# Optimization experiments

Measured on AMD Instinct MI355X. Metric: run time of the kernel, lower is better.

## Reference

```python
import jax, jax.numpy as jnp
import numpy as np

B, N_IN, N_HID, N_OUT, N_CLUST = 4096, 32, 128, 30000, 10000
BN_EPS = 1e-3  # scvi FCLayers uses BatchNorm1d(eps=0.001)


def setup_inputs() -> dict:
    key = jax.random.key(0)
    ks = jax.random.split(key, 4)
    z = jax.random.normal(ks[0], (B, N_IN), dtype=jnp.float32)
    W1 = jax.random.normal(ks[1], (N_HID, N_IN), dtype=jnp.float32) * 0.1
    b1 = jnp.zeros((N_HID,), dtype=jnp.float32)
    gamma = jnp.ones((N_HID,), dtype=jnp.float32)
    beta = jnp.zeros((N_HID,), dtype=jnp.float32)
    W2 = jax.random.normal(ks[2], (N_OUT, N_HID), dtype=jnp.float32) * 0.05
    b2 = jnp.zeros((N_OUT,), dtype=jnp.float32)
    # 3 introns per cluster, sorted cluster ids; first intron of each cluster
    intron_clusters = (jnp.arange(N_OUT, dtype=jnp.int32) // 3).astype(jnp.int32)
    first_indices = (jnp.arange(N_CLUST, dtype=jnp.int32) * 3).astype(jnp.int32)
    return {"z": z, "W1": W1, "b1": b1, "gamma": gamma, "beta": beta,
            "W2": W2, "b2": b2, "intron_clusters": intron_clusters,
            "first_indices": first_indices}


def reference(z, W1, b1, gamma, beta, W2, b2, intron_clusters, first_indices):
    # FCLayers (1 layer, dropout=0): Linear -> BatchNorm1d (batch stats) -> ReLU
    h = z @ W1.T + b1                                   # [B, n_hidden]
    mu = jnp.mean(h, axis=0)
    var = jnp.var(h, axis=0)
    h = gamma * (h - mu) * jax.lax.rsqrt(var + BN_EPS) + beta
    h = jax.nn.relu(h)
    # second_part Linear
    potentials = h @ W2.T + b2                          # [B, n_output]
    # pin first intron of each cluster to 0 (scatter-zero mask)
    potentials = potentials.at[:, first_indices].set(0.0)
    p_u = jnp.exp(potentials)                           # [B, n_output]
    # sparse cluster_summation @ p_u.T  ==  segment sum over introns per cluster
    cluster_sums = jax.ops.segment_sum(p_u.T, intron_clusters,
                                       num_segments=N_CLUST).T  # [B, n_clusters]
    # gather each intron's cluster sum and normalize (segment softmax)
    norm_factor = cluster_sums[:, intron_clusters]      # [B, n_output]
    return p_u / norm_factor
```

## Files before the change

### kernel.cpp

```cpp
#include <hip/hip_runtime.h>
#include <hip/hip_bf16.h>


typedef float  floatx4 __attribute__((ext_vector_type(4)));
typedef __bf16 bf16x8  __attribute__((ext_vector_type(8)));
typedef __bf16 bf16x4  __attribute__((ext_vector_type(4)));

struct F3 { float x, y, z; };

#define GLOBAL_AS __attribute__((address_space(1)))
#define LDS_AS    __attribute__((address_space(3)))

__device__ __forceinline__ void async16(void* lds, const void* g) {
    __builtin_amdgcn_global_load_lds((const GLOBAL_AS void*)g, (LDS_AS void*)lds, 16, 0, 0);
}

__global__ __launch_bounds__(256) void k_hidden_cvt(const float* __restrict__ z,
                                                    const float* __restrict__ W1,
                                                    const float* __restrict__ b1,
                                                    float* __restrict__ h,
                                                    float* __restrict__ stats,
                                                    const float* __restrict__ w2,
                                                    __bf16* __restrict__ w2b) {
    const int bid = blockIdx.x;
    const int tid = threadIdx.x;
    if (bid >= 256) {
        const int i  = (bid - 256) * 256 + tid;
        const int rp = i >> 4;
        const int c  = i & 15;
        const int nb = rp >> 5, n = rp & 31;
        const int src = nb * 48 + 3 * (n & 15) + 1 + (n >> 4);
        const float* s = w2 + (size_t)src * 128 + c * 8;
        floatx4 v0 = *(const floatx4*)s;
        floatx4 v1 = *(const floatx4*)(s + 4);
        bf16x8 o;
        o[0] = (__bf16)v0[0]; o[1] = (__bf16)v0[1]; o[2] = (__bf16)v0[2]; o[3] = (__bf16)v0[3];
        o[4] = (__bf16)v1[0]; o[5] = (__bf16)v1[1]; o[6] = (__bf16)v1[2]; o[7] = (__bf16)v1[3];
        *(bf16x8*)(w2b + (size_t)rp * 128 + c * 8) = o;
        return;
    }
    __shared__ float sW1[128 * 33];
    __shared__ float sz[16 * 32];
    __shared__ float red[256];
    const int rb = bid * 16;
    for (int i = tid; i < 128 * 32; i += 256) sW1[(i >> 5) * 33 + (i & 31)] = W1[i];
    for (int i = tid; i < 16 * 32; i += 256) sz[i] = z[rb * 32 + i];
    __syncthreads();
    const int col = tid & 127, rh = tid >> 7;
    const float bias = b1[col];
    float lsum = 0.f, lsq = 0.f;
    for (int r = rh; r < 16; r += 2) {
        float acc = bias;
#pragma unroll
        for (int k = 0; k < 32; ++k) acc += sz[r * 32 + k] * sW1[col * 33 + k];
        h[(rb + r) * 128 + col] = acc;
        lsum += acc; lsq += acc * acc;
    }
    red[tid] = lsum; __syncthreads();
    if (rh == 0) atomicAdd(&stats[col], red[col] + red[col + 128]);
    __syncthreads();
    red[tid] = lsq; __syncthreads();
    if (rh == 0) atomicAdd(&stats[128 + col], red[col] + red[col + 128]);
}

__global__ __launch_bounds__(256) void k_norm(const float* __restrict__ h,
                                              const float* __restrict__ stats,
                                              const float* __restrict__ gamma,
                                              const float* __restrict__ beta,
                                              __bf16* __restrict__ hb) {
    const int idx = blockIdx.x * 256 + threadIdx.x;
    const int c0  = (idx * 4) & 127;
    floatx4 v = *(const floatx4*)(h + (size_t)idx * 4);
    bf16x4 o;
#pragma unroll
    for (int j = 0; j < 4; ++j) {
        const int col = c0 + j;
        const float mu  = stats[col] * (1.0f / 4096.0f);
        const float var = stats[128 + col] * (1.0f / 4096.0f) - mu * mu;
        const float sc  = gamma[col] * rsqrtf(var + 1e-3f);
        const float sh  = beta[col] - mu * sc;
        o[j] = (__bf16)fmaxf(v[j] * sc + sh, 0.0f);
    }
    *(bf16x4*)(hb + (size_t)idx * 4) = o;
}

__global__ __launch_bounds__(256, 3) void k_main(const __bf16* __restrict__ hb,
                                                 const __bf16* __restrict__ w2b,
                                                 const float* __restrict__ b2,
                                                 float* __restrict__ out) {
    __shared__ __align__(16) char smem[32768 + 2 * 8192];
    char* smemA = smem;
    const int tid    = threadIdx.x;
    const int rowblk = blockIdx.x & 31;
    const int slot   = blockIdx.x >> 5;
    const int row0   = rowblk * 128;

    {
        const char* g = (const char*)(hb + (size_t)row0 * 128);
#pragma unroll
        for (int it = 0; it < 8; ++it) {
            int L = it * 256 + tid;
            int row = L >> 4, c = L & 15;
            int gc = (c & 8) | ((c ^ row) & 7);
            async16(smemA + L * 16, g + (row * 16 + gc) * 16);
        }
    }
    auto stageB = [&](char* dst, int nb) {
        const char* g = (const char*)(w2b + (size_t)nb * 32 * 128);
#pragma unroll
        for (int it = 0; it < 2; ++it) {
            int L = it * 256 + tid;
            int n = L >> 4, c = L & 15;
            int gc = (c & 8) | ((c ^ n) & 7);
            async16(dst + L * 16, g + (n * 16 + gc) * 16);
        }
    };
    stageB(smem + 32768, slot);

    const int lane = tid & 63, w = tid >> 6;
    const int quad = lane >> 4, lr = lane & 15;
    const int cnt = (624 - slot) / 24 + 1;
    __syncthreads();

    for (int i = 0; i < cnt; ++i) {
        const int nblk = slot + 24 * i;
        char* bcur  = smem + 32768 + ((i & 1) << 13);
        char* bnext = smem + 32768 + ((~i & 1) << 13);
        if (i + 1 < cnt) stageB(bnext, nblk + 24);

        const int cb = nblk * 48 + 3 * lr;
        const float bb1 = b2[cb + 1];
        const float bb2 = b2[cb + 2];

        const floatx4 z4 = {0.f, 0.f, 0.f, 0.f};
        floatx4 acc[2][2] = {{z4, z4}, {z4, z4}};
#pragma unroll
        for (int ks = 0; ks < 4; ++ks) {
            const int cg = ks * 4 + quad;
            bf16x8 a[2], b[2];
#pragma unroll
            for (int s = 0; s < 2; ++s) {
                int r  = w * 32 + s * 16 + lr;
                int ch = (cg & 8) | ((cg ^ r) & 7);
                a[s] = *(const bf16x8*)(smemA + r * 256 + ch * 16);
            }
#pragma unroll
            for (int t = 0; t < 2; ++t) {
                int n  = t * 16 + lr;
                int ch = (cg & 8) | ((cg ^ n) & 7);
                b[t] = *(const bf16x8*)(bcur + n * 256 + ch * 16);
            }
#pragma unroll
            for (int s = 0; s < 2; ++s)
#pragma unroll
                for (int t = 0; t < 2; ++t)
                    acc[s][t] = __builtin_amdgcn_mfma_f32_16x16x32_bf16(a[s], b[t], acc[s][t], 0, 0, 0);
        }

#pragma unroll
        for (int s = 0; s < 2; ++s) {
#pragma unroll
            for (int r = 0; r < 4; ++r) {
                int m = row0 + w * 32 + s * 16 + quad * 4 + r;
                float v1  = __expf(acc[s][0][r] + bb1);
                float v2  = __expf(acc[s][1][r] + bb2);
                float inv = __builtin_amdgcn_rcpf(1.0f + v1 + v2);
                F3 o; o.x = inv; o.y = v1 * inv; o.z = v2 * inv;
                *(F3*)(out + (size_t)m * 30000 + cb) = o;
            }
        }
        __syncthreads();
    }
}

extern "C" void kernel_launch(void* const* d_in, const int* in_sizes, int n_in,
                              void* d_out, int out_size, void* d_ws, size_t ws_size,
                              hipStream_t stream) {
    const float* z     = (const float*)d_in[0];
    const float* W1    = (const float*)d_in[1];
    const float* b1    = (const float*)d_in[2];
    const float* gamma = (const float*)d_in[3];
    const float* beta  = (const float*)d_in[4];
    const float* W2    = (const float*)d_in[5];
    const float* b2    = (const float*)d_in[6];
    float* out = (float*)d_out;

    char* ws = (char*)d_ws;
    float*  h     = (float*)ws;
    __bf16* hb    = (__bf16*)(ws + (2u << 20));
    __bf16* w2b   = (__bf16*)(ws + (3u << 20));
    float*  stats = (float*)(ws + (11u << 20));

    hipMemsetAsync(stats, 0, 256 * sizeof(float), stream);
    k_hidden_cvt<<<1506, 256, 0, stream>>>(z, W1, b1, h, stats, W2, w2b);
    k_norm<<<512, 256, 0, stream>>>(h, stats, gamma, beta, hb);
    k_main<<<768, 256, 0, stream>>>(hb, w2b, b2, out);
}
```

Baseline: 564.6 us.

## Replace persistent double-buffered B loop with one-shot 2D grid tiles

The main GEMM+softmax kernel drops its persistent loop over 24 slots with double-buffered W2 tiles. It now launches a 32x313 grid where each block loads its A tile and a 64-row W2 tile once, computes two cluster groups, and writes the output. This removes the per-iteration barrier and lets many more blocks hide store latency, but each block has to reload the 32KB A tile, which adds L2 traffic and launch overhead. The last column handles only one group.

```diff
diff --git a/kernel.cpp b/kernel.cpp
--- a/kernel.cpp
+++ b/kernel.cpp
@@ -88,12 +88,14 @@
                                                  const __bf16* __restrict__ w2b,
                                                  const float* __restrict__ b2,
                                                  float* __restrict__ out) {
-    __shared__ __align__(16) char smem[32768 + 2 * 8192];
+    __shared__ __align__(16) char smem[49152];
     char* smemA = smem;
+    char* smemB = smem + 32768;
     const int tid    = threadIdx.x;
-    const int rowblk = blockIdx.x & 31;
-    const int slot   = blockIdx.x >> 5;
+    const int rowblk = blockIdx.x;
+    const int y      = blockIdx.y;
     const int row0   = rowblk * 128;
+    const int ulim   = (y == 312) ? 1 : 2;
 
     {
         const char* g = (const char*)(hb + (size_t)row0 * 128);
@@ -105,71 +107,79 @@
             async16(smemA + L * 16, g + (row * 16 + gc) * 16);
         }
     }
-    auto stageB = [&](char* dst, int nb) {
-        const char* g = (const char*)(w2b + (size_t)nb * 32 * 128);
-#pragma unroll
-        for (int it = 0; it < 2; ++it) {
+    {
+        const char* g = (const char*)(w2b + (size_t)y * 64 * 128);
+#pragma unroll
+        for (int it = 0; it < 4; ++it) {
             int L = it * 256 + tid;
             int n = L >> 4, c = L & 15;
             int gc = (c & 8) | ((c ^ n) & 7);
-            async16(dst + L * 16, g + (n * 16 + gc) * 16);
-        }
-    };
-    stageB(smem + 32768, slot);
+            int nn = (n < 32 * ulim) ? n : (n - 32);
+            async16(smemB + L * 16, g + (nn * 16 + gc) * 16);
+        }
+    }
 
     const int lane = tid & 63, w = tid >> 6;
     const int quad = lane >> 4, lr = lane & 15;
-    const int cnt = (624 - slot) / 24 + 1;
+    const int cb0 = y * 96 + 3 * lr;
+    float bb1[2], bb2[2];
+    bb1[0] = b2[cb0 + 1]; bb2[0] = b2[cb0 + 2];
+    if (ulim > 1) { bb1[1] = b2[cb0 + 49]; bb2[1] = b2[cb0 + 50]; }
+    else          { bb1[1] = 0.f;          bb2[1] = 0.f; }
     __syncthreads();
 
-    for (int i = 0; i < cnt; ++i) {
-        const int nblk = slot + 24 * i;
-        char* bcur  = smem + 32768 + ((i & 1) << 13);
-        char* bnext = smem + 32768 + ((~i & 1) << 13);
-        if (i + 1 < cnt) stageB(bnext, nblk + 24);
-
-        const int cb = nblk * 48 + 3 * lr;
-        const float bb1 = b2[cb + 1];
-        const float bb2 = b2[cb + 2];
-
-        const floatx4 z4 = {0.f, 0.f, 0.f, 0.f};
-        floatx4 acc[2][2] = {{z4, z4}, {z4, z4}};
-#pragma unroll
-        for (int ks = 0; ks < 4; ++ks) {
-            const int cg = ks * 4 + quad;
-            bf16x8 a[2], b[2];
-#pragma unroll
-            for (int s = 0; s < 2; ++s) {
-                int r  = w * 32 + s * 16 + lr;
-                int ch = (cg & 8) | ((cg ^ r) & 7);
-                a[s] = *(const bf16x8*)(smemA + r * 256 + ch * 16);
+    const floatx4 z4 = {0.f, 0.f, 0.f, 0.f};
+    floatx4 acc[2][2][2];
+#pragma unroll
+    for (int s = 0; s < 2; ++s)
+#pragma unroll
+        for (int u = 0; u < 2; ++u)
+#pragma unroll
+            for (int t = 0; t < 2; ++t) acc[s][u][t] = z4;
+
+#pragma unroll
+    for (int ks = 0; ks < 4; ++ks) {
+        const int cg = ks * 4 + quad;
+        bf16x8 a[2], b[2][2];
+#pragma unroll
+        for (int s = 0; s < 2; ++s) {
+            int r  = w * 32 + s * 16 + lr;
+            int ch = (cg & 8) | ((cg ^ r) & 7);
+            a[s] = *(const bf16x8*)(smemA + r * 256 + ch * 16);
+        }
+#pragma unroll
+        for (int u = 0; u < 2; ++u)
+#pragma unroll
+            for (int t = 0; t < 2; ++t) {
+                int n  = u * 32 + t * 16 + lr;
+                int ch = (cg & 8) | ((cg ^ n) & 7);
+                b[u][t] = *(const bf16x8*)(smemB + n * 256 + ch * 16);
             }
 #pragma unroll
-            for (int t = 0; t < 2; ++t) {
-                int n  = t * 16 + lr;
-                int ch = (cg & 8) | ((cg ^ n) & 7);
-                b[t] = *(const bf16x8*)(bcur + n * 256 + ch * 16);
+        for (int s = 0; s < 2; ++s)
+#pragma unroll
+            for (int u = 0; u < 2; ++u)
+#pragma unroll
+                for (int t = 0; t < 2; ++t)
+                    acc[s][u][t] = __builtin_amdgcn_mfma_f32_16x16x32_bf16(a[s], b[u][t], acc[s][u][t], 0, 0, 0);
+    }
+
+#pragma unroll
+    for (int s = 0; s < 2; ++s) {
+#pragma unroll
+        for (int u = 0; u < 2; ++u) {
+            if (u < ulim) {
+#pragma unroll
+                for (int r = 0; r < 4; ++r) {
+                    int m = row0 + w * 32 + s * 16 + quad * 4 + r;
+                    float v1  = __expf(acc[s][u][0][r] + bb1[u]);
+                    float v2  = __expf(acc[s][u][1][r] + bb2[u]);
+                    float inv = __builtin_amdgcn_rcpf(1.0f + v1 + v2);
+                    F3 o; o.x = inv; o.y = v1 * inv; o.z = v2 * inv;
+                    *(F3*)(out + (size_t)m * 30000 + cb0 + u * 48) = o;
+                }
             }
-#pragma unroll
-            for (int s = 0; s < 2; ++s)
-#pragma unroll
-                for (int t = 0; t < 2; ++t)
-                    acc[s][t] = __builtin_amdgcn_mfma_f32_16x16x32_bf16(a[s], b[t], acc[s][t], 0, 0, 0);
-        }
-
-#pragma unroll
-        for (int s = 0; s < 2; ++s) {
-#pragma unroll
-            for (int r = 0; r < 4; ++r) {
-                int m = row0 + w * 32 + s * 16 + quad * 4 + r;
-                float v1  = __expf(acc[s][0][r] + bb1);
-                float v2  = __expf(acc[s][1][r] + bb2);
-                float inv = __builtin_amdgcn_rcpf(1.0f + v1 + v2);
-                F3 o; o.x = inv; o.y = v1 * inv; o.z = v2 * inv;
-                *(F3*)(out + (size_t)m * 30000 + cb) = o;
-            }
-        }
-        __syncthreads();
+        }
     }
 }
 
@@ -194,5 +204,6 @@
     hipMemsetAsync(stats, 0, 256 * sizeof(float), stream);
     k_hidden_cvt<<<1506, 256, 0, stream>>>(z, W1, b1, h, stats, W2, w2b);
     k_norm<<<512, 256, 0, stream>>>(h, stats, gamma, beta, hb);
-    k_main<<<768, 256, 0, stream>>>(hb, w2b, b2, out);
-}
+    dim3 grid(32, 313);
+    k_main<<<grid, 256, 0, stream>>>(hb, w2b, b2, out);
+}
```

Result: faster. 542.5 us (-3.9%).
